# Kernel optimization log

Measured on AMD Instinct MI355X. Metric: run time of the kernel, lower is better.

The kernel has to match this reference:

```python
import jax, jax.numpy as jnp
import numpy as np

INF = 1000000000000000.0  # 1e15, matches the TF source

B, H, S, D = 4, 16, 1024, 64


def setup_inputs() -> dict:
    key = jax.random.key(0)
    kq, kk, kv, kp = jax.random.split(key, 4)
    q = jax.random.normal(kq, (B, H, S, D), dtype=jnp.float32)
    k = jax.random.normal(kk, (B, H, S, D), dtype=jnp.float32)
    v = jax.random.normal(kv, (B, H, S, D), dtype=jnp.float32)
    # pad_mask: 1 = masked-out key position, broadcast over heads and queries
    pad_mask = jax.random.randint(kp, (B, 1, 1, S), 0, 2, dtype=jnp.int32)
    # look_ahead_mask: 1 above the diagonal (future positions masked)
    look_ahead_mask = jnp.triu(jnp.ones((S, S), dtype=jnp.int32), k=1)[None, None]
    return {"q": q, "k": k, "v": v, "pad_mask": pad_mask,
            "look_ahead_mask": look_ahead_mask}


def reference(q, k, v, pad_mask, look_ahead_mask):
    d_model = jnp.float32(q.shape[3])
    # scores: (B, H, Sq, Sk)
    score_logits = jnp.einsum("bhqd,bhkd->bhqk", q, k) / jnp.sqrt(d_model)
    if pad_mask is not None:
        score_logits = score_logits + pad_mask.astype(jnp.float32) * (-INF)
    if look_ahead_mask is not None:
        score_logits = score_logits + look_ahead_mask.astype(jnp.float32) * (-INF)
    attention_weights = jax.nn.softmax(score_logits, axis=-1)
    context_vector = jnp.einsum("bhqk,bhkd->bhqd", attention_weights, v)
    return (context_vector, attention_weights)
```

## Files before the change

### kernel.cpp

```cpp
#include <hip/hip_runtime.h>
#include <stdint.h>

#define S 1024
#define D 64
#define TQ 16
#define KT 128
#define NKT 8
#define NEG (-1e15f)
#define SCALE 0.125f

#define WB_STRIDE 1048
#define KB_STRIDE 72
#define VT_STRIDE 136
#define QS_STRIDE 72

typedef __bf16 bf16x8 __attribute__((ext_vector_type(8)));
typedef float f32x4 __attribute__((ext_vector_type(4)));
typedef unsigned short ushort_t;

__device__ __forceinline__ unsigned short f2b(float f) {
  union { float f; uint32_t u; } c; c.f = f;
  uint32_t u = c.u;
  return (unsigned short)((u + 0x7fffu + ((u >> 16) & 1u)) >> 16);
}
__device__ __forceinline__ float b2f(uint32_t u) {
  union { uint32_t u; float f; } c; c.u = u << 16;
  return c.f;
}

__device__ __forceinline__ void barrier_lds_only() {
  asm volatile("s_waitcnt lgkmcnt(0)" ::: "memory");
  __builtin_amdgcn_s_barrier();
  __builtin_amdgcn_sched_barrier(0);
}

__global__ __launch_bounds__(256) void prep_k_kernel(
    const float* __restrict__ Kg, ushort_t* __restrict__ Kb)
{
  const size_t idx = ((size_t)blockIdx.x * 256 + threadIdx.x) * 8;
  float4 a = *(const float4*)(Kg + idx);
  float4 b = *(const float4*)(Kg + idx + 4);
  ushort_t tmp[8];
  tmp[0]=f2b(a.x); tmp[1]=f2b(a.y); tmp[2]=f2b(a.z); tmp[3]=f2b(a.w);
  tmp[4]=f2b(b.x); tmp[5]=f2b(b.y); tmp[6]=f2b(b.z); tmp[7]=f2b(b.w);
  *(uint4*)(Kb + idx) = *(const uint4*)tmp;
}

__global__ __launch_bounds__(256) void prep_vt_kernel(
    const float* __restrict__ Vg, ushort_t* __restrict__ Vt)
{
  __shared__ __align__(16) ushort_t lvt[D * QS_STRIDE];
  const int t = threadIdx.x;
  const int bh = blockIdx.x >> 4;
  const int j0 = (blockIdx.x & 15) << 6;

  {
    const int j = t >> 2, sd = (t & 3) << 4;
    const float* src = Vg + ((size_t)bh * S + j0 + j) * D + sd;
#pragma unroll
    for (int c = 0; c < 4; ++c) {
      float4 f = *(const float4*)(src + (c << 2));
      lvt[(sd + (c << 2) + 0) * QS_STRIDE + j] = f2b(f.x);
      lvt[(sd + (c << 2) + 1) * QS_STRIDE + j] = f2b(f.y);
      lvt[(sd + (c << 2) + 2) * QS_STRIDE + j] = f2b(f.z);
      lvt[(sd + (c << 2) + 3) * QS_STRIDE + j] = f2b(f.w);
    }
  }
  __syncthreads();
  {
    const int d = t >> 2, sj = (t & 3) << 4;
    ushort_t tmp[16];
#pragma unroll
    for (int c = 0; c < 4; ++c)
      *(ushort4*)&tmp[c << 2] = *(const ushort4*)&lvt[d * QS_STRIDE + sj + (c << 2)];
    ushort_t* dst = Vt + ((size_t)bh * D + d) * S + j0 + sj;
    *(uint4*)dst = *(const uint4*)&tmp[0];
    *(uint4*)(dst + 8) = *(const uint4*)&tmp[8];
  }
}

__global__ __launch_bounds__(512, 6) void attn_kernel(
    const float* __restrict__ Qg, const ushort_t* __restrict__ Kb,
    const ushort_t* __restrict__ Vtb, const int* __restrict__ PADg,
    float* __restrict__ OCTX, float* __restrict__ OW)
{
  __shared__ __align__(16) ushort_t wb[TQ * WB_STRIDE];
  __shared__ __align__(16) ushort_t ub[KT * KB_STRIDE];

  const int t  = threadIdx.x;
  const int w  = t >> 6;
  const int l  = t & 63;
  const int la = l & 15;
  const int lb = l >> 4;

  const int hwblk = blockIdx.x;
  const int slot  = hwblk >> 3;
  const int bh    = ((hwblk & 7) << 3) + (slot >> 6);
  const int qt    = slot & 63;
  const int qr0   = qt << 4;

  const size_t head = (size_t)bh * S * D;
  const int* pp = PADg + (size_t)(bh >> 4) * S;

  bf16x8 aq0, aq1;
  {
    const float* qrow = Qg + head + (size_t)(qr0 + la) * D + (lb << 3);
    float4 q00 = *(const float4*)(qrow);
    float4 q01 = *(const float4*)(qrow + 4);
    float4 q10 = *(const float4*)(qrow + 32);
    float4 q11 = *(const float4*)(qrow + 36);
    ushort_t a0[8], a1[8];
    a0[0]=f2b(q00.x); a0[1]=f2b(q00.y); a0[2]=f2b(q00.z); a0[3]=f2b(q00.w);
    a0[4]=f2b(q01.x); a0[5]=f2b(q01.y); a0[6]=f2b(q01.z); a0[7]=f2b(q01.w);
    a1[0]=f2b(q10.x); a1[1]=f2b(q10.y); a1[2]=f2b(q10.z); a1[3]=f2b(q10.w);
    a1[4]=f2b(q11.x); a1[5]=f2b(q11.y); a1[6]=f2b(q11.z); a1[7]=f2b(q11.w);
    aq0 = *(const bf16x8*)a0;
    aq1 = *(const bf16x8*)a1;
  }

  {
    const int kr = l >> 2;
    const int ko = (l & 3) << 4;
    const int rowg = (w << 4) + kr;
    const ushort_t* ksrc = Kb + head + (size_t)rowg * D + ko;
    ushort_t* kdst = &ub[rowg * KB_STRIDE + ko];
    const int j0 = w << 4;
    uint4 kra[2], krb[2];
    kra[0] = *(const uint4*)(ksrc);
    krb[0] = *(const uint4*)(ksrc + 8);
    kra[1] = *(const uint4*)(ksrc + (size_t)(KT * D));
    krb[1] = *(const uint4*)(ksrc + (size_t)(KT * D) + 8);
#pragma unroll
    for (int kt = 0; kt < NKT; ++kt) {
      *(uint4*)kdst = kra[kt & 1];
      *(uint4*)(kdst + 8) = krb[kt & 1];
      if (kt + 2 < NKT) {
        const ushort_t* ns = ksrc + (size_t)(kt + 2) * (KT * D);
        kra[kt & 1] = *(const uint4*)(ns);
        krb[kt & 1] = *(const uint4*)(ns + 8);
      }
      f32x4 acc = {0.f, 0.f, 0.f, 0.f};
      bf16x8 b0 = *(const bf16x8*)&ub[(j0 + la) * KB_STRIDE + (lb << 3)];
      acc = __builtin_amdgcn_mfma_f32_16x16x32_bf16(aq0, b0, acc, 0, 0, 0);
      bf16x8 b1 = *(const bf16x8*)&ub[(j0 + la) * KB_STRIDE + 32 + (lb << 3)];
      acc = __builtin_amdgcn_mfma_f32_16x16x32_bf16(aq1, b1, acc, 0, 0, 0);
#pragma unroll
      for (int i = 0; i < 4; ++i)
        wb[((lb << 2) + i) * WB_STRIDE + kt * KT + j0 + la] = f2b(acc[i]);
    }
  }
  barrier_lds_only();

  const int jh = w >> 2;
  const int d0 = (w & 3) << 4;
  const int vr = l >> 2;
  const int vo = (l & 3) << 4;
  const ushort_t* vsrc = Vtb + (size_t)bh * (D * S) + (size_t)(d0 + vr) * S
                        + jh * 64 + vo;
  ushort_t* vdst = &ub[(d0 + vr) * VT_STRIDE + jh * 64 + vo];
  uint4 vra[2], vrb[2];
  vra[0] = *(const uint4*)(vsrc);
  vrb[0] = *(const uint4*)(vsrc + 8);
  vra[1] = *(const uint4*)(vsrc + KT);
  vrb[1] = *(const uint4*)(vsrc + KT + 8);

#pragma unroll
  for (int rr = 0; rr < 2; ++rr) {
    const int r  = (w << 1) + rr;
    const int qr = qr0 + r;
    float lg[16];
    float m = -3.0e38f;
#pragma unroll
    for (int ii = 0; ii < 8; ++ii) {
      const int j = (l << 1) + (ii << 7);
      uint32_t pr = *(const uint32_t*)&wb[r * WB_STRIDE + j];
      int2 pv = *(const int2*)&pp[j];
      float l0 = b2f(pr & 0xffffu) * SCALE + (pv.x ? NEG : 0.0f) + ((j     > qr) ? NEG : 0.0f);
      float l1 = b2f(pr >> 16)     * SCALE + (pv.y ? NEG : 0.0f) + ((j + 1 > qr) ? NEG : 0.0f);
      lg[2 * ii] = l0; lg[2 * ii + 1] = l1;
      m = fmaxf(m, fmaxf(l0, l1));
    }
#pragma unroll
    for (int off = 32; off > 0; off >>= 1) m = fmaxf(m, __shfl_xor(m, off, 64));
    float sum = 0.f;
#pragma unroll
    for (int x = 0; x < 16; ++x) { lg[x] = __expf(lg[x] - m); sum += lg[x]; }
#pragma unroll
    for (int off = 32; off > 0; off >>= 1) sum += __shfl_xor(sum, off, 64);
    const float inv = 1.0f / sum;
    float* orow = OW + (size_t)(bh * S + qr) * S;
#pragma unroll
    for (int ii = 0; ii < 8; ++ii) {
      const int j = (l << 1) + (ii << 7);
      float w0 = lg[2 * ii] * inv, w1 = lg[2 * ii + 1] * inv;
      *(uint32_t*)&wb[r * WB_STRIDE + j] = ((uint32_t)f2b(w1) << 16) | (uint32_t)f2b(w0);
      unsigned long long uw = ((unsigned long long)__float_as_uint(w1) << 32)
                            | (unsigned long long)__float_as_uint(w0);
      __builtin_nontemporal_store(uw, (unsigned long long*)&orow[j]);
    }
  }
  barrier_lds_only();

  f32x4 cacc = {0.f, 0.f, 0.f, 0.f};
  {
#pragma unroll
    for (int kt = 0; kt < NKT; ++kt) {
      *(uint4*)vdst = vra[kt & 1];
      *(uint4*)(vdst + 8) = vrb[kt & 1];
      if (kt + 2 < NKT) {
        const ushort_t* nv = vsrc + (kt + 2) * KT;
        vra[kt & 1] = *(const uint4*)(nv);
        vrb[kt & 1] = *(const uint4*)(nv + 8);
      }
#pragma unroll
      for (int ks = 0; ks < 2; ++ks) {
        const int jt = jh * 64 + ks * 32;
        bf16x8 af = *(const bf16x8*)&wb[la * WB_STRIDE + kt * KT + jt + (lb << 3)];
        bf16x8 bf = *(const bf16x8*)&ub[(d0 + la) * VT_STRIDE + jt + (lb << 3)];
        cacc = __builtin_amdgcn_mfma_f32_16x16x32_bf16(af, bf, cacc, 0, 0, 0);
      }
    }
  }
  barrier_lds_only();

  float* pbuf = (float*)ub;
  if (w >= 4) {
#pragma unroll
    for (int i = 0; i < 4; ++i)
      pbuf[(w - 4) * 320 + ((lb << 2) + i) * 20 + la] = cacc[i];
  }
  barrier_lds_only();
  if (w < 4) {
#pragma unroll
    for (int i = 0; i < 4; ++i) {
      const int qrow = (lb << 2) + i;
      __builtin_nontemporal_store(
          cacc[i] + pbuf[w * 320 + qrow * 20 + la],
          &OCTX[((size_t)(bh * S) + qr0 + qrow) * D + d0 + la]);
    }
  }
}

extern "C" void kernel_launch(void* const* d_in, const int* in_sizes, int n_in,
                              void* d_out, int out_size, void* d_ws, size_t ws_size,
                              hipStream_t stream) {
  const float* q   = (const float*)d_in[0];
  const float* k   = (const float*)d_in[1];
  const float* v   = (const float*)d_in[2];
  const int*   pad = (const int*)d_in[3];
  float* ctx  = (float*)d_out;
  float* wout = (float*)d_out + (size_t)4 * 16 * S * D;

  ushort_t* Kb  = (ushort_t*)d_ws;
  ushort_t* Vtb = (ushort_t*)d_ws + (size_t)4 * 16 * S * D;

  prep_k_kernel <<<dim3(2048), dim3(256), 0, stream>>>(k, Kb);
  prep_vt_kernel<<<dim3(1024), dim3(256), 0, stream>>>(v, Vtb);
  attn_kernel   <<<dim3(4096), dim3(512), 0, stream>>>(q, Kb, Vtb, pad, ctx, wout);
}
```

Measured before the change: 380.3 us.

## Merge K/V prep kernels, deepen K/V prefetch to three stages, use exp2 softmax

```diff
diff --git a/kernel.cpp b/kernel.cpp
--- a/kernel.cpp
+++ b/kernel.cpp
@@ -7,7 +7,7 @@
 #define KT 128
 #define NKT 8
 #define NEG (-1e15f)
-#define SCALE 0.125f
+#define SCALE2 0.180336880f
 
 #define WB_STRIDE 1048
 #define KB_STRIDE 72
@@ -34,26 +34,25 @@
   __builtin_amdgcn_sched_barrier(0);
 }
 
-__global__ __launch_bounds__(256) void prep_k_kernel(
-    const float* __restrict__ Kg, ushort_t* __restrict__ Kb)
-{
-  const size_t idx = ((size_t)blockIdx.x * 256 + threadIdx.x) * 8;
-  float4 a = *(const float4*)(Kg + idx);
-  float4 b = *(const float4*)(Kg + idx + 4);
-  ushort_t tmp[8];
-  tmp[0]=f2b(a.x); tmp[1]=f2b(a.y); tmp[2]=f2b(a.z); tmp[3]=f2b(a.w);
-  tmp[4]=f2b(b.x); tmp[5]=f2b(b.y); tmp[6]=f2b(b.z); tmp[7]=f2b(b.w);
-  *(uint4*)(Kb + idx) = *(const uint4*)tmp;
-}
-
-__global__ __launch_bounds__(256) void prep_vt_kernel(
-    const float* __restrict__ Vg, ushort_t* __restrict__ Vt)
+__global__ __launch_bounds__(256) void prep_kv_kernel(
+    const float* __restrict__ Kg, const float* __restrict__ Vg,
+    ushort_t* __restrict__ Kb, ushort_t* __restrict__ Vt)
 {
   __shared__ __align__(16) ushort_t lvt[D * QS_STRIDE];
   const int t = threadIdx.x;
-  const int bh = blockIdx.x >> 4;
-  const int j0 = (blockIdx.x & 15) << 6;
-
+  if (blockIdx.x < 2048) {
+    const size_t idx = ((size_t)blockIdx.x * 256 + t) * 8;
+    float4 a = *(const float4*)(Kg + idx);
+    float4 b = *(const float4*)(Kg + idx + 4);
+    ushort_t tmp[8];
+    tmp[0]=f2b(a.x); tmp[1]=f2b(a.y); tmp[2]=f2b(a.z); tmp[3]=f2b(a.w);
+    tmp[4]=f2b(b.x); tmp[5]=f2b(b.y); tmp[6]=f2b(b.z); tmp[7]=f2b(b.w);
+    *(uint4*)(Kb + idx) = *(const uint4*)tmp;
+    return;
+  }
+  const int bid = blockIdx.x - 2048;
+  const int bh = bid >> 4;
+  const int j0 = (bid & 15) << 6;
   {
     const int j = t >> 2, sd = (t & 3) << 4;
     const float* src = Vg + ((size_t)bh * S + j0 + j) * D + sd;
@@ -79,7 +78,7 @@
   }
 }
 
-__global__ __launch_bounds__(512, 6) void attn_kernel(
+__global__ __launch_bounds__(512, 4) void attn_kernel(
     const float* __restrict__ Qg, const ushort_t* __restrict__ Kb,
     const ushort_t* __restrict__ Vtb, const int* __restrict__ PADg,
     float* __restrict__ OCTX, float* __restrict__ OW)
@@ -125,19 +124,22 @@
     const ushort_t* ksrc = Kb + head + (size_t)rowg * D + ko;
     ushort_t* kdst = &ub[rowg * KB_STRIDE + ko];
     const int j0 = w << 4;
-    uint4 kra[2], krb[2];
+    uint4 kra[3], krb[3];
     kra[0] = *(const uint4*)(ksrc);
     krb[0] = *(const uint4*)(ksrc + 8);
     kra[1] = *(const uint4*)(ksrc + (size_t)(KT * D));
     krb[1] = *(const uint4*)(ksrc + (size_t)(KT * D) + 8);
+    kra[2] = *(const uint4*)(ksrc + (size_t)(2 * KT * D));
+    krb[2] = *(const uint4*)(ksrc + (size_t)(2 * KT * D) + 8);
 #pragma unroll
     for (int kt = 0; kt < NKT; ++kt) {
-      *(uint4*)kdst = kra[kt & 1];
-      *(uint4*)(kdst + 8) = krb[kt & 1];
-      if (kt + 2 < NKT) {
-        const ushort_t* ns = ksrc + (size_t)(kt + 2) * (KT * D);
-        kra[kt & 1] = *(const uint4*)(ns);
-        krb[kt & 1] = *(const uint4*)(ns + 8);
+      const int s = kt % 3;
+      *(uint4*)kdst = kra[s];
+      *(uint4*)(kdst + 8) = krb[s];
+      if (kt + 3 < NKT) {
+        const ushort_t* ns = ksrc + (size_t)(kt + 3) * (KT * D);
+        kra[s] = *(const uint4*)(ns);
+        krb[s] = *(const uint4*)(ns + 8);
       }
       f32x4 acc = {0.f, 0.f, 0.f, 0.f};
       bf16x8 b0 = *(const bf16x8*)&ub[(j0 + la) * KB_STRIDE + (lb << 3)];
@@ -158,11 +160,13 @@
   const ushort_t* vsrc = Vtb + (size_t)bh * (D * S) + (size_t)(d0 + vr) * S
                         + jh * 64 + vo;
   ushort_t* vdst = &ub[(d0 + vr) * VT_STRIDE + jh * 64 + vo];
-  uint4 vra[2], vrb[2];
+  uint4 vra[3], vrb[3];
   vra[0] = *(const uint4*)(vsrc);
   vrb[0] = *(const uint4*)(vsrc + 8);
   vra[1] = *(const uint4*)(vsrc + KT);
   vrb[1] = *(const uint4*)(vsrc + KT + 8);
+  vra[2] = *(const uint4*)(vsrc + 2 * KT);
+  vrb[2] = *(const uint4*)(vsrc + 2 * KT + 8);
 
 #pragma unroll
   for (int rr = 0; rr < 2; ++rr) {
@@ -175,8 +179,8 @@
       const int j = (l << 1) + (ii << 7);
       uint32_t pr = *(const uint32_t*)&wb[r * WB_STRIDE + j];
       int2 pv = *(const int2*)&pp[j];
-      float l0 = b2f(pr & 0xffffu) * SCALE + (pv.x ? NEG : 0.0f) + ((j     > qr) ? NEG : 0.0f);
-      float l1 = b2f(pr >> 16)     * SCALE + (pv.y ? NEG : 0.0f) + ((j + 1 > qr) ? NEG : 0.0f);
+      float l0 = b2f(pr & 0xffffu) * SCALE2 + (pv.x ? NEG : 0.0f) + ((j     > qr) ? NEG : 0.0f);
+      float l1 = b2f(pr >> 16)     * SCALE2 + (pv.y ? NEG : 0.0f) + ((j + 1 > qr) ? NEG : 0.0f);
       lg[2 * ii] = l0; lg[2 * ii + 1] = l1;
       m = fmaxf(m, fmaxf(l0, l1));
     }
@@ -184,7 +188,7 @@
     for (int off = 32; off > 0; off >>= 1) m = fmaxf(m, __shfl_xor(m, off, 64));
     float sum = 0.f;
 #pragma unroll
-    for (int x = 0; x < 16; ++x) { lg[x] = __expf(lg[x] - m); sum += lg[x]; }
+    for (int x = 0; x < 16; ++x) { lg[x] = exp2f(lg[x] - m); sum += lg[x]; }
 #pragma unroll
     for (int off = 32; off > 0; off >>= 1) sum += __shfl_xor(sum, off, 64);
     const float inv = 1.0f / sum;
@@ -205,12 +209,13 @@
   {
 #pragma unroll
     for (int kt = 0; kt < NKT; ++kt) {
-      *(uint4*)vdst = vra[kt & 1];
-      *(uint4*)(vdst + 8) = vrb[kt & 1];
-      if (kt + 2 < NKT) {
-        const ushort_t* nv = vsrc + (kt + 2) * KT;
-        vra[kt & 1] = *(const uint4*)(nv);
-        vrb[kt & 1] = *(const uint4*)(nv + 8);
+      const int s = kt % 3;
+      *(uint4*)vdst = vra[s];
+      *(uint4*)(vdst + 8) = vrb[s];
+      if (kt + 3 < NKT) {
+        const ushort_t* nv = vsrc + (kt + 3) * KT;
+        vra[s] = *(const uint4*)(nv);
+        vrb[s] = *(const uint4*)(nv + 8);
       }
 #pragma unroll
       for (int ks = 0; ks < 2; ++ks) {
@@ -254,7 +259,6 @@
   ushort_t* Kb  = (ushort_t*)d_ws;
   ushort_t* Vtb = (ushort_t*)d_ws + (size_t)4 * 16 * S * D;
 
-  prep_k_kernel <<<dim3(2048), dim3(256), 0, stream>>>(k, Kb);
-  prep_vt_kernel<<<dim3(1024), dim3(256), 0, stream>>>(v, Vtb);
+  prep_kv_kernel<<<dim3(3072), dim3(256), 0, stream>>>(k, v, Kb, Vtb);
   attn_kernel   <<<dim3(4096), dim3(512), 0, stream>>>(q, Kb, Vtb, pad, ctx, wout);
 }
```

Result: no change. 385.9 us (+1.5%).
